# Performance work log

Measured on AMD Instinct MI355X. Metric: run time of the kernel, lower is better.

Reference implementation:

```python
import jax, jax.numpy as jnp
import numpy as np

INPUT_DIM = 1024; HID = 512; DSTATE = 64; EXPAND = 2; HDIM = 32; NHEAD = 8; DFF = 1024
DIN = EXPAND * HID          # 1024 inner dim
NH = DIN // HDIM            # 32 heads
G = 1; DCONV = 4            # ngroups, depthwise conv kernel
CONV_DIM = DIN + 2 * G * DSTATE          # 1152 (x, B, C go through conv)
DPROJ = 2 * DIN + 2 * G * DSTATE + NH    # 2208 (z, xBC, dt)
B = 2; L = 4096


def rmsnorm(x, w, eps=1e-5):
    return x * jax.lax.rsqrt(jnp.mean(x * x, axis=-1, keepdims=True) + eps) * w


def layernorm(x, w, b, eps=1e-5):
    m = jnp.mean(x, axis=-1, keepdims=True)
    v = jnp.mean((x - m) ** 2, axis=-1, keepdims=True)
    return (x - m) * jax.lax.rsqrt(v + eps) * w + b


def mamba_block(x, Wi, cw, cb, dtb, Alog, Dp, nw, Wo):
    # Mamba-2 style selective scan block (SISO, ngroups=1)
    Bb, Ln, _ = x.shape
    zxbcdt = x @ Wi                                   # [B,L,DPROJ]
    z = zxbcdt[..., :DIN]
    xBC = zxbcdt[..., DIN:DIN + CONV_DIM]
    dt = zxbcdt[..., DIN + CONV_DIM:]                 # [B,L,NH]
    # causal depthwise conv1d + silu
    xBC = jnp.transpose(xBC, (0, 2, 1))               # [B,C,L]
    xBC = jax.lax.conv_general_dilated(xBC, cw, (1,), [(DCONV - 1, 0)],
                                       feature_group_count=CONV_DIM) + cb[None, :, None]
    xBC = jax.nn.silu(jnp.transpose(xBC, (0, 2, 1)))
    xs = xBC[..., :DIN].reshape(Bb, Ln, NH, HDIM)     # [B,L,H,P]
    Bm = xBC[..., DIN:DIN + DSTATE]                   # [B,L,N]
    Cm = xBC[..., DIN + DSTATE:]                      # [B,L,N]
    dt = jax.nn.softplus(dt + dtb)                    # [B,L,H]
    decay = jnp.exp(dt * (-jnp.exp(Alog)))            # [B,L,H]
    dtx = dt[..., None] * xs                          # [B,L,H,P]

    def step(h, inp):
        dec, dx, Bt, Ct = inp                         # [B,H],[B,H,P],[B,N],[B,N]
        h = h * dec[:, :, None, None] + dx[..., None] * Bt[:, None, None, :]
        return h, jnp.einsum('bhpn,bn->bhp', h, Ct)

    h0 = jnp.zeros((Bb, NH, HDIM, DSTATE), x.dtype)
    _, ys = jax.lax.scan(step, h0, (jnp.moveaxis(decay, 1, 0), jnp.moveaxis(dtx, 1, 0),
                                    jnp.moveaxis(Bm, 1, 0), jnp.moveaxis(Cm, 1, 0)))
    y = jnp.moveaxis(ys, 0, 1) + Dp[None, None, :, None] * xs
    y = y.reshape(Bb, Ln, DIN)
    return rmsnorm(y * jax.nn.silu(z), nw) @ Wo       # gated RMSNorm + out proj


def transformer_layer(x, Wqkv, bqkv, Wo, bo, W1, b1, W2, b2, ln1w, ln1b, ln2w, ln2b):
    Bb, Ln, Dm = x.shape
    hd = Dm // NHEAD
    qkv = x @ Wqkv + bqkv
    q, k, v = jnp.split(qkv, 3, axis=-1)
    sp = lambda t: t.reshape(Bb, Ln, NHEAD, hd).transpose(0, 2, 1, 3)
    q, k, v = sp(q), sp(k), sp(v)
    att = jax.nn.softmax(jnp.einsum('bhqd,bhkd->bhqk', q, k) / np.float32(np.sqrt(hd)), axis=-1)
    o = jnp.einsum('bhqk,bhkd->bhqd', att, v).transpose(0, 2, 1, 3).reshape(Bb, Ln, Dm)
    x = layernorm(x + o @ Wo + bo, ln1w, ln1b)
    ff = jax.nn.gelu(x @ W1 + b1, approximate=False) @ W2 + b2
    return layernorm(x + ff, ln2w, ln2b)


def setup_inputs() -> dict:
    key = jax.random.key(0)
    ks = iter(jax.random.split(key, 64))
    w = lambda shape, s=0.02: jax.random.normal(next(ks), shape, jnp.float32) * s
    d = {}
    d['x'] = jax.random.normal(next(ks), (B, L, INPUT_DIM), jnp.float32)
    d['Wp'] = w((INPUT_DIM, HID)); d['bp'] = jnp.zeros((HID,), jnp.float32)
    for p in ('m1', 'm2'):
        d[p + '_Wi'] = w((HID, DPROJ))
        d[p + '_cw'] = w((CONV_DIM, 1, DCONV), 0.2)
        d[p + '_cb'] = jnp.zeros((CONV_DIM,), jnp.float32)
        d[p + '_dtb'] = jnp.log(jnp.expm1(jax.random.uniform(next(ks), (NH,), jnp.float32, 0.001, 0.1)))
        d[p + '_Alog'] = jnp.log(jax.random.uniform(next(ks), (NH,), jnp.float32, 1.0, 16.0))
        d[p + '_D'] = jnp.ones((NH,), jnp.float32)
        d[p + '_nw'] = jnp.ones((DIN,), jnp.float32)
        d[p + '_Wo'] = w((DIN, HID))
    d['n1_w'] = jnp.ones((HID,), jnp.float32); d['n2_w'] = jnp.ones((HID,), jnp.float32)
    d['ds_w'] = w((HID, HID, 3)); d['ds_b'] = jnp.zeros((HID,), jnp.float32)
    d['t_Wqkv'] = w((HID, 3 * HID)); d['t_bqkv'] = jnp.zeros((3 * HID,), jnp.float32)
    d['t_Wo'] = w((HID, HID)); d['t_bo'] = jnp.zeros((HID,), jnp.float32)
    d['t_W1'] = w((HID, DFF)); d['t_b1'] = jnp.zeros((DFF,), jnp.float32)
    d['t_W2'] = w((DFF, HID)); d['t_b2'] = jnp.zeros((HID,), jnp.float32)
    d['t_ln1w'] = jnp.ones((HID,), jnp.float32); d['t_ln1b'] = jnp.zeros((HID,), jnp.float32)
    d['t_ln2w'] = jnp.ones((HID,), jnp.float32); d['t_ln2b'] = jnp.zeros((HID,), jnp.float32)
    d['on_w'] = jnp.ones((HID,), jnp.float32); d['on_b'] = jnp.zeros((HID,), jnp.float32)
    return d


def reference(x, Wp, bp,
              m1_Wi, m1_cw, m1_cb, m1_dtb, m1_Alog, m1_D, m1_nw, m1_Wo,
              m2_Wi, m2_cw, m2_cb, m2_dtb, m2_Alog, m2_D, m2_nw, m2_Wo,
              n1_w, n2_w, ds_w, ds_b,
              t_Wqkv, t_bqkv, t_Wo, t_bo, t_W1, t_b1, t_W2, t_b2,
              t_ln1w, t_ln1b, t_ln2w, t_ln2b, on_w, on_b):
    x = x @ Wp + bp
    x = rmsnorm(mamba_block(x, m1_Wi, m1_cw, m1_cb, m1_dtb, m1_Alog, m1_D, m1_nw, m1_Wo) + x, n1_w)
    x = rmsnorm(mamba_block(x, m2_Wi, m2_cw, m2_cb, m2_dtb, m2_Alog, m2_D, m2_nw, m2_Wo) + x, n2_w)
    xt = jnp.transpose(x, (0, 2, 1))                  # [B,HID,L]
    xt = jax.lax.conv_general_dilated(xt, ds_w, (2,), [(1, 1)]) + ds_b[None, :, None]
    x = jnp.transpose(xt, (0, 2, 1))                  # [B,L/2,HID]
    x = transformer_layer(x, t_Wqkv, t_bqkv, t_Wo, t_bo, t_W1, t_b1, t_W2, t_b2,
                          t_ln1w, t_ln1b, t_ln2w, t_ln2b)
    return layernorm(x, on_w, on_b)
```

## Files before the change

### kernel.cpp

```cpp
#include <hip/hip_runtime.h>
#include <math.h>

#define DIN_   1024
#define DSTATE_ 64
#define NH_    32
#define HDIM_  32
#define CONVD_ 1152
#define DPROJ_ 2208
#define HID_   512
#define LSEQ_  4096
#define BB_    2
#define LT_    2048
#define NHEAD_ 8
#define HD_    64
#define DFF_   1024
#define LC_    256
#define NC_    16
#define NS_    4
#define KTS_   (LT_ / 64 / NS_)

typedef __attribute__((ext_vector_type(8))) short bf16x8;
typedef __attribute__((ext_vector_type(4))) short s16x4;
typedef __attribute__((ext_vector_type(4))) float f32x4;

__device__ __forceinline__ float siluf(float x) { return x / (1.f + __expf(-x)); }

__device__ __forceinline__ short f2b(float f) {
  union { float f; unsigned u; } v; v.f = f;
  unsigned r = (v.u + 0x7fffu + ((v.u >> 16) & 1u)) >> 16;
  return (short)r;
}

__device__ __forceinline__ short f2bt(float f) {
  union { float f; unsigned u; } v; v.f = f;
  return (short)(v.u >> 16);
}

__device__ __forceinline__ float b2f(short s) {
  union { unsigned u; float f; } v; v.u = ((unsigned)(unsigned short)s) << 16;
  return v.f;
}

__device__ __forceinline__ void gload16(const short* g, short* lds_base) {
#if __has_builtin(__builtin_amdgcn_global_load_lds)
  __builtin_amdgcn_global_load_lds((const __attribute__((address_space(1))) void*)g,
                                   (__attribute__((address_space(3))) void*)lds_base, 16, 0, 0);
#else
  int l = threadIdx.x & 63;
  ((bf16x8*)lds_base)[l] = *(const bf16x8*)g;
#endif
}

__device__ __forceinline__ void xcd_swz(int& bx, int& by, int& bz) {
  int nbx = gridDim.x, nby = gridDim.y;
  int nwg = nbx * nby * gridDim.z;
  int orig = (blockIdx.z * nby + blockIdx.y) * nbx + blockIdx.x;
  int q = nwg >> 3, r = nwg & 7;
  int xcd = orig & 7, lin = orig >> 3;
  int wg = (xcd < r ? xcd * (q + 1) : r * (q + 1) + (xcd - r) * q) + lin;
  bx = wg % nbx; wg /= nbx;
  by = wg % nby;
  bz = wg / nby;
}

__global__ void ec_f2b(const float* __restrict__ in, short* __restrict__ out, int n8)
{
  int i = blockIdx.x * 256 + threadIdx.x;
  if (i >= n8) return;
  const float4* p = (const float4*)(in + (size_t)i * 8);
  float4 a = p[0], b = p[1];
  bf16x8 o;
  o[0] = f2b(a.x); o[1] = f2b(a.y); o[2] = f2b(a.z); o[3] = f2b(a.w);
  o[4] = f2b(b.x); o[5] = f2b(b.y); o[6] = f2b(b.z); o[7] = f2b(b.w);
  *(bf16x8*)(out + (size_t)i * 8) = o;
}

__global__ __launch_bounds__(256) void ec_w2bt(const float* __restrict__ W,
                                               short* __restrict__ Wt, int K, int N)
{
  __shared__ float t[32][33];
  int k0 = blockIdx.x * 32, n0 = blockIdx.y * 32;
  int tx = threadIdx.x & 31, ty = threadIdx.x >> 5;
#pragma unroll
  for (int i = 0; i < 32; i += 8) t[ty + i][tx] = W[(size_t)(k0 + ty + i) * N + n0 + tx];
  __syncthreads();
#pragma unroll
  for (int i = 0; i < 32; i += 8) Wt[(size_t)(n0 + ty + i) * K + k0 + tx] = f2b(t[tx][ty + i]);
}

__global__ void ec_dswt(const float* __restrict__ w, short* __restrict__ wt)
{
  int idx = blockIdx.x * 256 + threadIdx.x;
  if (idx >= HID_ * 1536) return;
  int o = idx / 1536, r = idx % 1536;
  int k = r >> 9, i = r & 511;
  wt[idx] = f2b(w[((size_t)o * HID_ + i) * 3 + k]);
}

__global__ void ec_cwt(const float* __restrict__ cw, float* __restrict__ cwt)
{
  int idx = blockIdx.x * 256 + threadIdx.x;
  if (idx >= CONVD_ * 4) return;
  int j = idx / CONVD_, c = idx % CONVD_;
  cwt[idx] = cw[c * 4 + j];
}

__global__ __launch_bounds__(256) void ec_gemm16b(
    const short* __restrict__ A, const short* __restrict__ Wt,
    const float* __restrict__ bias, const float* __restrict__ res,
    float* __restrict__ Cf, short* __restrict__ Ch,
    int M, int N, int K, int act, int lda, long Az, int Mz)
{
  __shared__ short As_[2][4096];
  __shared__ short Bs_[2][4096];
  int bxi, byi, bzi;
  xcd_swz(bxi, byi, bzi);
  A += (size_t)bzi * Az;
  const int mz = bzi * Mz;
  const int tid = threadIdx.x;
  const int l = tid & 63, w = tid >> 6;
  const int m0 = byi * 64, n0 = bxi * 64;
  const int wm = (w >> 1) * 32, wn = (w & 1) * 32;
  const int lr = l & 15, lk = l >> 4;
  const int srow = w * 8 + (l >> 3);
  const int scol = ((l & 7) ^ (l >> 3)) * 8;
  const int rs0 = ((0 * 4 + lk) ^ (lr & 7)) * 8;
  const int rs1 = ((1 * 4 + lk) ^ (lr & 7)) * 8;

  f32x4 acc[2][2];
#pragma unroll
  for (int i = 0; i < 2; ++i)
#pragma unroll
    for (int j = 0; j < 2; ++j) acc[i][j] = f32x4{0.f, 0.f, 0.f, 0.f};

#pragma unroll
  for (int q = 0; q < 2; ++q) {
    int r = q * 32 + srow;
    const short* ga = A + (size_t)(m0 + r) * lda + scol;
    int rb = n0 + r; if (rb > N - 1) rb = N - 1;
    const short* gb = Wt + (size_t)rb * K + scol;
    gload16(ga, &As_[0][(q * 32 + w * 8) * 64]);
    gload16(gb, &Bs_[0][(q * 32 + w * 8) * 64]);
  }

  const int KT = K >> 6;
  for (int kt = 0; kt < KT; ++kt) {
    __syncthreads();
    if (kt + 1 < KT) {
      int k0 = (kt + 1) << 6;
      int nb = (kt + 1) & 1;
#pragma unroll
      for (int q = 0; q < 2; ++q) {
        int r = q * 32 + srow;
        const short* ga = A + (size_t)(m0 + r) * lda + k0 + scol;
        int rb = n0 + r; if (rb > N - 1) rb = N - 1;
        const short* gb = Wt + (size_t)rb * K + k0 + scol;
        gload16(ga, &As_[nb][(q * 32 + w * 8) * 64]);
        gload16(gb, &Bs_[nb][(q * 32 + w * 8) * 64]);
      }
    }
    int cb = kt & 1;
#pragma unroll
    for (int ksub = 0; ksub < 2; ++ksub) {
      const int rs = ksub ? rs1 : rs0;
      bf16x8 af[2], bfv[2];
#pragma unroll
      for (int mf = 0; mf < 2; ++mf)
        af[mf] = *(const bf16x8*)&As_[cb][(wm + mf * 16 + lr) * 64 + rs];
#pragma unroll
      for (int nf = 0; nf < 2; ++nf)
        bfv[nf] = *(const bf16x8*)&Bs_[cb][(wn + nf * 16 + lr) * 64 + rs];
#pragma unroll
      for (int mf = 0; mf < 2; ++mf)
#pragma unroll
        for (int nf = 0; nf < 2; ++nf)
          acc[mf][nf] = __builtin_amdgcn_mfma_f32_16x16x32_bf16(af[mf], bfv[nf], acc[mf][nf], 0, 0, 0);
    }
  }

#pragma unroll
  for (int mf = 0; mf < 2; ++mf)
#pragma unroll
    for (int nf = 0; nf < 2; ++nf)
#pragma unroll
      for (int r = 0; r < 4; ++r) {
        int m = mz + m0 + wm + mf * 16 + lk * 4 + r;
        int n = n0 + wn + nf * 16 + lr;
        if (n < N) {
          float v = acc[mf][nf][r];
          if (bias) v += bias[n];
          if (act == 1) v = 0.5f * v * (1.f + erff(v * 0.70710678118f));
          else if (act == 2 && n < HID_) v *= 0.125f;
          if (res) v += res[(size_t)m * N + n];
          if (Cf) Cf[(size_t)m * N + n] = v;
          if (Ch) Ch[(size_t)m * N + n] = f2b(v);
        }
      }
}

static inline void gemm16b(hipStream_t s, const short* A, const short* Wt, const float* bias,
                           const float* res, float* Cf, short* Ch, int M, int N, int K, int act) {
  dim3 g((N + 63) / 64, M / 64), b(256);
  ec_gemm16b<<<g, b, 0, s>>>(A, Wt, bias, res, Cf, Ch, M, N, K, act, K, 0, 0);
}

__global__ __launch_bounds__(512) void ec_dsfix(
    const short* __restrict__ x16, const short* __restrict__ wt,
    const float* __restrict__ bias, float* __restrict__ dsf, short* __restrict__ ds16)
{
  const int b = blockIdx.x, o = threadIdx.x;
  float v = bias[o];
#pragma unroll
  for (int k = 1; k < 3; ++k) {
    const short* xr = x16 + ((size_t)b * LSEQ_ + (k - 1)) * HID_;
    const short* wr = wt + (size_t)o * 1536 + k * 512;
    for (int i = 0; i < 512; i += 4) {
      s16x4 xv = *(const s16x4*)(xr + i);
      s16x4 wv = *(const s16x4*)(wr + i);
      v += b2f(xv[0]) * b2f(wv[0]) + b2f(xv[1]) * b2f(wv[1])
         + b2f(xv[2]) * b2f(wv[2]) + b2f(xv[3]) * b2f(wv[3]);
    }
  }
  dsf[(size_t)b * LT_ * HID_ + o] = v;
  ds16[(size_t)b * LT_ * HID_ + o] = f2b(v);
}

__global__ __launch_bounds__(256) void ec_conv1d_silu(
    const short* __restrict__ zx16, const float* __restrict__ cwt,
    const float* __restrict__ cb, short* __restrict__ xbc16,
    short* __restrict__ B16, short* __restrict__ C16)
{
  int idx = blockIdx.x * 256 + threadIdx.x;
  const int NG = CONVD_ / 4;
  if (idx >= BB_ * LSEQ_ * NG) return;
  int cg = idx % NG;
  int row = idx / NG;
  int l = row & (LSEQ_ - 1);
  int c0 = cg * 4;
  float4 cbv = *(const float4*)(cb + c0);
  float a0 = cbv.x, a1 = cbv.y, a2 = cbv.z, a3 = cbv.w;
#pragma unroll
  for (int j = 0; j < 4; ++j) {
    int ll = l - 3 + j;
    if (ll >= 0) {
      s16x4 xv = *(const s16x4*)(zx16 + (size_t)(row + ll - l) * DPROJ_ + DIN_ + c0);
      float4 wv = *(const float4*)(cwt + j * CONVD_ + c0);
      a0 += b2f(xv[0]) * wv.x;
      a1 += b2f(xv[1]) * wv.y;
      a2 += b2f(xv[2]) * wv.z;
      a3 += b2f(xv[3]) * wv.w;
    }
  }
  a0 = siluf(a0); a1 = siluf(a1); a2 = siluf(a2); a3 = siluf(a3);
  s16x4 pk; pk[0] = f2b(a0); pk[1] = f2b(a1); pk[2] = f2b(a2); pk[3] = f2b(a3);
  *(s16x4*)(xbc16 + (size_t)row * CONVD_ + c0) = pk;
  if (c0 >= DIN_) {
    int col = c0 - DIN_;
    if (col < 64) *(s16x4*)(B16 + (size_t)row * 64 + col) = pk;
    else          *(s16x4*)(C16 + (size_t)row * 64 + col - 64) = pk;
  }
}

__global__ __launch_bounds__(256) void ec_ssd_cumsum(
    const short* __restrict__ zx16, const float* __restrict__ dtb,
    const float* __restrict__ Alog, float* __restrict__ dts,
    float* __restrict__ lp, float* __restrict__ Pc)
{
  const int c = blockIdx.x, b = blockIdx.y, hg = blockIdx.z;
  const int t = threadIdx.x;
  const int lane = t & 63, wv = t >> 6;
  const size_t row = (size_t)b * LSEQ_ + (size_t)c * LC_ + t;
  const int h0 = hg * 8;
  __shared__ float wsum[4][8];

  bf16x8 dv = *(const bf16x8*)(zx16 + row * DPROJ_ + (DIN_ + CONVD_) + h0);
  float dt[8], cs[8];
#pragma unroll
  for (int j = 0; j < 8; ++j) {
    float x = b2f(dv[j]) + dtb[h0 + j];
    float sp = (x > 20.f) ? x : log1pf(__expf(x));
    dt[j] = sp;
    cs[j] = sp;
  }
#pragma unroll
  for (int d = 1; d < 64; d <<= 1) {
#pragma unroll
    for (int j = 0; j < 8; ++j) {
      float o = __shfl_up(cs[j], d, 64);
      if (lane >= d) cs[j] += o;
    }
  }
  if (lane == 63)
#pragma unroll
    for (int j = 0; j < 8; ++j) wsum[wv][j] = cs[j];
  __syncthreads();
#pragma unroll
  for (int j = 0; j < 8; ++j) {
    float base = 0.f;
#pragma unroll
    for (int k = 0; k < 3; ++k) if (k < wv) base += wsum[k][j];
    cs[j] += base;
  }
#pragma unroll
  for (int j = 0; j < 8; ++j) {
    int h = h0 + j;
    float lpv = -expf(Alog[h]) * cs[j];
    dts[row * NH_ + h] = dt[j];
    lp[row * NH_ + h] = lpv;
    if (t == LC_ - 1) Pc[(b * NC_ + c) * NH_ + h] = expf(lpv);
  }
}

__global__ __launch_bounds__(64) void ec_vt(
    const short* __restrict__ xbc16, const float* __restrict__ dts, short* __restrict__ VT)
{
  const int h = blockIdx.x, c = blockIdx.y, b = blockIdx.z;
  const int l = threadIdx.x;
  const size_t rowB = (size_t)b * LSEQ_ + (size_t)c * LC_;
  const size_t vtbase = (size_t)((b * NC_ + c) * NH_ + h) * 32;
  __shared__ float tile[32][33];
  for (int tt = 0; tt < 8; ++tt) {
#pragma unroll
    for (int i = 0; i < 16; ++i) {
      int r = i * 2 + (l >> 5);
      size_t row = rowB + tt * 32 + r;
      tile[r][l & 31] = b2f(xbc16[row * CONVD_ + h * 32 + (l & 31)]) * dts[row * NH_ + h];
    }
    __syncthreads();
#pragma unroll
    for (int j = 0; j < 16; ++j) {
      int p = j * 2 + (l >> 5);
      VT[(vtbase + p) * 256 + tt * 32 + (l & 31)] = f2b(tile[l & 31][p]);
    }
    __syncthreads();
  }
}

__device__ __forceinline__ float* state_ptr(float* stbuf, int b, int c, int h, int e)
{
  return stbuf + ((size_t)((b * NC_ + c) * NH_ + h)) * 2048 + e;
}

__global__ __launch_bounds__(64) void ec_ssd_p1(
    const short* __restrict__ B16, const short* __restrict__ VT,
    const float* __restrict__ lp, float* __restrict__ stbuf)
{
  const int h = blockIdx.x, c = blockIdx.y, b = blockIdx.z;
  const int l = threadIdx.x, lr = l & 15, lk = l >> 4;
  const size_t rowB = (size_t)b * LSEQ_ + (size_t)c * LC_;
  const size_t vtbase = (size_t)((b * NC_ + c) * NH_ + h) * 32;
  __shared__ short BT[64][264];
  for (int i = 0; i < 4; ++i) {
    int t = i * 64 + l;
#pragma unroll
    for (int g = 0; g < 8; ++g) {
      bf16x8 v = *(const bf16x8*)&B16[(rowB + t) * 64 + g * 8];
#pragma unroll
      for (int j = 0; j < 8; ++j) BT[g * 8 + j][t] = v[j];
    }
  }
  __syncthreads();
  const float lpE = lp[(rowB + LC_ - 1) * NH_ + h];
  f32x4 acc[2][4];
#pragma unroll
  for (int i = 0; i < 2; ++i)
#pragma unroll
    for (int j = 0; j < 4; ++j) acc[i][j] = f32x4{0.f, 0.f, 0.f, 0.f};

  for (int ks = 0; ks < 8; ++ks) {
    float wv[8];
#pragma unroll
    for (int j = 0; j < 8; ++j) {
      int t = ks * 32 + lk * 8 + j;
      wv[j] = __expf(lpE - lp[(rowB + t) * NH_ + h]);
    }
    bf16x8 af[2];
#pragma unroll
    for (int mf = 0; mf < 2; ++mf) {
      bf16x8 v = *(const bf16x8*)&VT[(vtbase + mf * 16 + lr) * 256 + ks * 32 + lk * 8];
#pragma unroll
      for (int j = 0; j < 8; ++j) af[mf][j] = f2b(b2f(v[j]) * wv[j]);
    }
#pragma unroll
    for (int nf = 0; nf < 4; ++nf) {
      bf16x8 bf = *(const bf16x8*)&BT[nf * 16 + lr][ks * 32 + lk * 8];
#pragma unroll
      for (int mf = 0; mf < 2; ++mf)
        acc[mf][nf] = __builtin_amdgcn_mfma_f32_16x16x32_bf16(af[mf], bf, acc[mf][nf], 0, 0, 0);
    }
  }
#pragma unroll
  for (int mf = 0; mf < 2; ++mf)
#pragma unroll
    for (int nf = 0; nf < 4; ++nf)
#pragma unroll
      for (int r = 0; r < 4; ++r) {
        int p = mf * 16 + lk * 4 + r, n = nf * 16 + lr;
        *state_ptr(stbuf, b, c, h, p * 64 + n) = acc[mf][nf][r];
      }
}

__global__ __launch_bounds__(512) void ec_scan_p2(
    float* __restrict__ stbuf, const float* __restrict__ Pc)
{
  const int h = blockIdx.x, b = blockIdx.y;
  const int tid = threadIdx.x;
  const int e = (tid >> 4) * 64 + (tid & 15) * 4;
  float h0 = 0.f, h1 = 0.f, h2 = 0.f, h3 = 0.f;
  for (int c = 0; c < NC_; ++c) {
    float* ptr = state_ptr(stbuf, b, c, h, e);
    float4 S = *(float4*)ptr;
    *(float4*)ptr = make_float4(h0, h1, h2, h3);
    float P = Pc[(b * NC_ + c) * NH_ + h];
    h0 = h0 * P + S.x;
    h1 = h1 * P + S.y;
    h2 = h2 * P + S.z;
    h3 = h3 * P + S.w;
  }
}

__global__ __launch_bounds__(256) void ec_ssd_p3(
    const short* __restrict__ B16, const short* __restrict__ C16,
    const short* __restrict__ VT, const float* __restrict__ lp,
    const short* __restrict__ xbc16, const float* __restrict__ Dp,
    float* __restrict__ stbuf, short* __restrict__ y16)
{
  const int h = blockIdx.x, c = blockIdx.y, b = blockIdx.z;
  const int tid = threadIdx.x;
  const int w = tid >> 6, l = tid & 63, lr = l & 15, lk = l >> 4;
  const size_t rowB = (size_t)b * LSEQ_ + (size_t)c * LC_;
  const size_t vtbase = (size_t)((b * NC_ + c) * NH_ + h) * 32;
  __shared__ short hI[32][72];
  __shared__ short Pl[4][64][72];

  for (int i = tid; i < 2048; i += 256)
    hI[i >> 6][i & 63] = f2b(*state_ptr(stbuf, b, c, h, i));
  __syncthreads();

  const int t0 = w * 64;
  bf16x8 cf[4][2];
#pragma unroll
  for (int tf = 0; tf < 4; ++tf)
#pragma unroll
    for (int ks = 0; ks < 2; ++ks)
      cf[tf][ks] = *(const bf16x8*)&C16[(rowB + t0 + tf * 16 + lr) * 64 + ks * 32 + lk * 8];

  f32x4 Y[4][2];
#pragma unroll
  for (int i = 0; i < 4; ++i)
#pragma unroll
    for (int j = 0; j < 2; ++j) Y[i][j] = f32x4{0.f, 0.f, 0.f, 0.f};
#pragma unroll
  for (int nf = 0; nf < 2; ++nf)
#pragma unroll
    for (int ks = 0; ks < 2; ++ks) {
      bf16x8 hf = *(const bf16x8*)&hI[nf * 16 + lr][ks * 32 + lk * 8];
#pragma unroll
      for (int mf = 0; mf < 4; ++mf)
        Y[mf][nf] = __builtin_amdgcn_mfma_f32_16x16x32_bf16(cf[mf][ks], hf, Y[mf][nf], 0, 0, 0);
    }
#pragma unroll
  for (int mf = 0; mf < 4; ++mf)
#pragma unroll
    for (int r = 0; r < 4; ++r) {
      float e = __expf(lp[(rowB + t0 + mf * 16 + lk * 4 + r) * NH_ + h]);
      Y[mf][0][r] *= e;
      Y[mf][1][r] *= e;
    }
  float tlp[4];
#pragma unroll
  for (int tf = 0; tf < 4; ++tf)
    tlp[tf] = lp[(rowB + t0 + tf * 16 + lr) * NH_ + h];

  for (int st = 0; st <= w; ++st) {
    const int s0 = st * 64;
#pragma unroll
    for (int half = 0; half < 2; ++half) {
      f32x4 ST[2][4];
#pragma unroll
      for (int i = 0; i < 2; ++i)
#pragma unroll
        for (int j = 0; j < 4; ++j) ST[i][j] = f32x4{0.f, 0.f, 0.f, 0.f};
#pragma unroll
      for (int sf2 = 0; sf2 < 2; ++sf2) {
        int sf = half * 2 + sf2;
#pragma unroll
        for (int ks = 0; ks < 2; ++ks) {
          bf16x8 bfr = *(const bf16x8*)&B16[(rowB + s0 + sf * 16 + lr) * 64 + ks * 32 + lk * 8];
#pragma unroll
          for (int tf = 0; tf < 4; ++tf)
            ST[sf2][tf] = __builtin_amdgcn_mfma_f32_16x16x32_bf16(bfr, cf[tf][ks], ST[sf2][tf], 0, 0, 0);
        }
      }
#pragma unroll
      for (int sf2 = 0; sf2 < 2; ++sf2) {
        int sf = half * 2 + sf2;
        float slp[4];
#pragma unroll
        for (int r = 0; r < 4; ++r)
          slp[r] = lp[(rowB + s0 + sf * 16 + lk * 4 + r) * NH_ + h];
#pragma unroll
        for (int tf = 0; tf < 4; ++tf) {
          float pv[4];
#pragma unroll
          for (int r = 0; r < 4; ++r) {
            pv[r] = ST[sf2][tf][r] * __expf(tlp[tf] - slp[r]);
            if (st == w && (sf * 16 + lk * 4 + r) > (tf * 16 + lr)) pv[r] = 0.f;
          }
          union { float f; unsigned u; } q0, q1, q2, q3;
          q0.f = pv[0]; q1.f = pv[1]; q2.f = pv[2]; q3.f = pv[3];
          uint2 pk;
          pk.x = (q0.u >> 16) | (q1.u & 0xffff0000u);
          pk.y = (q2.u >> 16) | (q3.u & 0xffff0000u);
          *(uint2*)&Pl[w][tf * 16 + lr][sf * 16 + lk * 4] = pk;
        }
      }
    }
    __builtin_amdgcn_sched_barrier(0);
    asm volatile("s_waitcnt lgkmcnt(0)" ::: "memory");
    __builtin_amdgcn_sched_barrier(0);
#pragma unroll
    for (int ks = 0; ks < 2; ++ks) {
      bf16x8 vf[2];
#pragma unroll
      for (int nf = 0; nf < 2; ++nf)
        vf[nf] = *(const bf16x8*)&VT[(vtbase + nf * 16 + lr) * 256 + s0 + ks * 32 + lk * 8];
#pragma unroll
      for (int mf = 0; mf < 4; ++mf) {
        bf16x8 pf = *(const bf16x8*)&Pl[w][mf * 16 + lr][ks * 32 + lk * 8];
#pragma unroll
        for (int nf = 0; nf < 2; ++nf)
          Y[mf][nf] = __builtin_amdgcn_mfma_f32_16x16x32_bf16(pf, vf[nf], Y[mf][nf], 0, 0, 0);
      }
    }
  }
  const float Dh = Dp[h];
#pragma unroll
  for (int mf = 0; mf < 4; ++mf)
#pragma unroll
    for (int r = 0; r < 4; ++r) {
      size_t yrow = rowB + t0 + mf * 16 + lk * 4 + r;
#pragma unroll
      for (int nf = 0; nf < 2; ++nf) {
        float xv = b2f(xbc16[yrow * CONVD_ + h * 32 + nf * 16 + lr]);
        y16[yrow * DIN_ + h * 32 + nf * 16 + lr] = f2b(Y[mf][nf][r] + Dh * xv);
      }
    }
}

__global__ __launch_bounds__(256) void ec_gate_rms16(
    const short* __restrict__ y16, const short* __restrict__ zx16,
    const float* __restrict__ nw, short* __restrict__ out)
{
  const int row = blockIdx.x;
  const int c0 = threadIdx.x * 4;
  s16x4 yv = *(const s16x4*)(y16 + (size_t)row * DIN_ + c0);
  s16x4 zv = *(const s16x4*)(zx16 + (size_t)row * DPROJ_ + c0);
  float v[4]; float ss = 0.f;
#pragma unroll
  for (int j = 0; j < 4; ++j) {
    float t = b2f(yv[j]) * siluf(b2f(zv[j]));
    v[j] = t; ss += t * t;
  }
#pragma unroll
  for (int m = 32; m >= 1; m >>= 1) ss += __shfl_xor(ss, m, 64);
  __shared__ float buf[4];
  if ((threadIdx.x & 63) == 0) buf[threadIdx.x >> 6] = ss;
  __syncthreads();
  ss = buf[0] + buf[1] + buf[2] + buf[3];
  float scale = rsqrtf(ss / (float)DIN_ + 1e-5f);
  float4 wv = *(const float4*)(nw + c0);
  s16x4 ov;
  ov[0] = f2b(v[0] * scale * wv.x);
  ov[1] = f2b(v[1] * scale * wv.y);
  ov[2] = f2b(v[2] * scale * wv.z);
  ov[3] = f2b(v[3] * scale * wv.w);
  *(s16x4*)(out + (size_t)row * DIN_ + c0) = ov;
}

__global__ __launch_bounds__(128) void ec_rmsadd16(
    const short* __restrict__ a16, const float* __restrict__ bres,
    const float* __restrict__ w, float* __restrict__ out, short* __restrict__ out16)
{
  const int row = blockIdx.x;
  const int c0 = threadIdx.x * 4;
  s16x4 av = *(const s16x4*)(a16 + (size_t)row * HID_ + c0);
  float4 brv = *(const float4*)(bres + (size_t)row * HID_ + c0);
  float v[4]; float ss = 0.f;
  v[0] = b2f(av[0]) + brv.x; v[1] = b2f(av[1]) + brv.y;
  v[2] = b2f(av[2]) + brv.z; v[3] = b2f(av[3]) + brv.w;
#pragma unroll
  for (int j = 0; j < 4; ++j) ss += v[j] * v[j];
#pragma unroll
  for (int m = 32; m >= 1; m >>= 1) ss += __shfl_xor(ss, m, 64);
  __shared__ float buf[2];
  if ((threadIdx.x & 63) == 0) buf[threadIdx.x >> 6] = ss;
  __syncthreads();
  ss = buf[0] + buf[1];
  float scale = rsqrtf(ss / (float)HID_ + 1e-5f);
  float4 wv = *(const float4*)(w + c0);
  float o0 = v[0] * scale * wv.x, o1 = v[1] * scale * wv.y;
  float o2 = v[2] * scale * wv.z, o3 = v[3] * scale * wv.w;
  *(float4*)(out + (size_t)row * HID_ + c0) = make_float4(o0, o1, o2, o3);
  s16x4 ov; ov[0] = f2b(o0); ov[1] = f2b(o1); ov[2] = f2b(o2); ov[3] = f2b(o3);
  *(s16x4*)(out16 + (size_t)row * HID_ + c0) = ov;
}

__global__ __launch_bounds__(128) void ec_ln16(
    const float* __restrict__ in, const float* __restrict__ w,
    const float* __restrict__ bb, float* __restrict__ out, short* __restrict__ out16)
{
  const int row = blockIdx.x;
  const float* ir = in + (size_t)row * HID_;
  float v[4]; float s = 0.f, s2 = 0.f;
#pragma unroll
  for (int j = 0; j < 4; ++j) {
    int c = j * 128 + threadIdx.x;
    float t = ir[c];
    v[j] = t; s += t; s2 += t * t;
  }
#pragma unroll
  for (int m = 32; m >= 1; m >>= 1) { s += __shfl_xor(s, m, 64); s2 += __shfl_xor(s2, m, 64); }
  __shared__ float buf[4];
  if ((threadIdx.x & 63) == 0) { int wi = threadIdx.x >> 6; buf[wi * 2] = s; buf[wi * 2 + 1] = s2; }
  __syncthreads();
  s = buf[0] + buf[2]; s2 = buf[1] + buf[3];
  float mean = s / (float)HID_;
  float var = s2 / (float)HID_ - mean * mean;
  float inv = rsqrtf(var + 1e-5f);
#pragma unroll
  for (int j = 0; j < 4; ++j) {
    int c = j * 128 + threadIdx.x;
    float o = (v[j] - mean) * inv * w[c] + bb[c];
    out[(size_t)row * HID_ + c] = o;
    if (out16) out16[(size_t)row * HID_ + c] = f2b(o);
  }
}

__global__ __launch_bounds__(512) void ec_attn16(
    const short* __restrict__ qkv, short* __restrict__ Op, float2* __restrict__ ml)
{
  const int b = blockIdx.z & 1, split = blockIdx.z >> 1;
  const int h = blockIdx.y, qt = blockIdx.x;
  __shared__ short Kl[64 * 68];
  __shared__ short Vl[64 * 68];
  __shared__ short Pl[128 * 68];
  const int tid = threadIdx.x;
  const int l = tid & 63, w = tid >> 6;
  const int lr = l & 15, lk = l >> 4;

  const size_t qrow = (size_t)b * LT_ + qt * 128 + w * 16 + lr;
  bf16x8 qf[2];
  qf[0] = *(const bf16x8*)&qkv[qrow * 1536 + h * HD_ + lk * 8];
  qf[1] = *(const bf16x8*)&qkv[qrow * 1536 + h * HD_ + lk * 8 + 32];

  float mrun[4] = {-1e30f, -1e30f, -1e30f, -1e30f};
  float lsum[4] = {0.f, 0.f, 0.f, 0.f};
  f32x4 O[4];
#pragma unroll
  for (int df = 0; df < 4; ++df) O[df] = f32x4{0.f, 0.f, 0.f, 0.f};

  const int krow = tid >> 3, kcg = (tid & 7) * 8;
  const int vd = tid & 63, vw = tid >> 6;

  for (int kt = split * KTS_; kt < (split + 1) * KTS_; ++kt) {
    const size_t krbase = (size_t)b * LT_ + kt * 64;
    {
      const short* kp = &qkv[(krbase + krow) * 1536 + HID_ + h * HD_ + kcg];
      *(bf16x8*)&Kl[krow * 68 + kcg] = *(const bf16x8*)kp;
    }
#pragma unroll
    for (int kk = 0; kk < 2; ++kk) {
      int key0 = vw * 8 + kk * 4;
      s16x4 pk;
#pragma unroll
      for (int j = 0; j < 4; ++j)
        pk[j] = qkv[(krbase + key0 + j) * 1536 + 2 * HID_ + h * HD_ + vd];
      *(s16x4*)&Vl[vd * 68 + key0] = pk;
    }
    __syncthreads();

    f32x4 S[4];
#pragma unroll
    for (int nf = 0; nf < 4; ++nf) S[nf] = f32x4{0.f, 0.f, 0.f, 0.f};
#pragma unroll
    for (int ks = 0; ks < 2; ++ks)
#pragma unroll
      for (int nf = 0; nf < 4; ++nf) {
        bf16x8 kb = *(const bf16x8*)&Kl[(nf * 16 + lr) * 68 + ks * 32 + lk * 8];
        S[nf] = __builtin_amdgcn_mfma_f32_16x16x32_bf16(qf[ks], kb, S[nf], 0, 0, 0);
      }

    int ok = 1;
#pragma unroll
    for (int nf = 0; nf < 4; ++nf)
#pragma unroll
      for (int r = 0; r < 4; ++r)
        ok &= (S[nf][r] <= mrun[r] + 8.f);
    if (!__all(ok)) {
      float fr[4];
#pragma unroll
      for (int r = 0; r < 4; ++r) {
        float mt = fmaxf(fmaxf(S[0][r], S[1][r]), fmaxf(S[2][r], S[3][r]));
        mt = fmaxf(mt, __shfl_xor(mt, 1));
        mt = fmaxf(mt, __shfl_xor(mt, 2));
        mt = fmaxf(mt, __shfl_xor(mt, 4));
        mt = fmaxf(mt, __shfl_xor(mt, 8));
        float mn = fmaxf(mrun[r], mt);
        fr[r] = __expf(mrun[r] - mn);
        mrun[r] = mn;
        lsum[r] *= fr[r];
      }
#pragma unroll
      for (int df = 0; df < 4; ++df) {
        O[df][0] *= fr[0]; O[df][1] *= fr[1]; O[df][2] *= fr[2]; O[df][3] *= fr[3];
      }
    }
#pragma unroll
    for (int nf = 0; nf < 4; ++nf)
#pragma unroll
      for (int r = 0; r < 4; ++r) {
        float p = __expf(S[nf][r] - mrun[r]);
        lsum[r] += p;
        Pl[(w * 16 + lk * 4 + r) * 68 + nf * 16 + lr] = f2bt(p);
      }

#pragma unroll
    for (int ks = 0; ks < 2; ++ks) {
      bf16x8 pa = *(const bf16x8*)&Pl[(w * 16 + lr) * 68 + ks * 32 + lk * 8];
#pragma unroll
      for (int df = 0; df < 4; ++df) {
        bf16x8 vb = *(const bf16x8*)&Vl[(df * 16 + lr) * 68 + ks * 32 + lk * 8];
        O[df] = __builtin_amdgcn_mfma_f32_16x16x32_bf16(pa, vb, O[df], 0, 0, 0);
      }
    }
    __syncthreads();
  }

#pragma unroll
  for (int r = 0; r < 4; ++r) {
    lsum[r] += __shfl_xor(lsum[r], 1);
    lsum[r] += __shfl_xor(lsum[r], 2);
    lsum[r] += __shfl_xor(lsum[r], 4);
    lsum[r] += __shfl_xor(lsum[r], 8);
  }
  const size_t sstride = (size_t)BB_ * NHEAD_ * LT_;
  const size_t obase = (size_t)split * sstride + ((size_t)b * NHEAD_ + h) * LT_ + qt * 128 + w * 16;
#pragma unroll
  for (int df = 0; df < 4; ++df)
#pragma unroll
    for (int r = 0; r < 4; ++r)
      Op[(obase + lk * 4 + r) * 64 + df * 16 + lr] = f2b(O[df][r]);
  if (lr == 0)
#pragma unroll
    for (int r = 0; r < 4; ++r)
      ml[obase + lk * 4 + r] = make_float2(mrun[r], lsum[r]);
}

__global__ __launch_bounds__(256) void ec_attn_comb(
    const short* __restrict__ Op, const float2* __restrict__ ml, short* __restrict__ out)
{
  const int qt = blockIdx.x, h = blockIdx.y, b = blockIdx.z;
  const int r = threadIdx.x >> 2, c0 = (threadIdx.x & 3) * 16;
  const int qrow = qt * 64 + r;
  const size_t sstride = (size_t)BB_ * NHEAD_ * LT_;
  const size_t rb = ((size_t)b * NHEAD_ + h) * LT_ + qrow;
  float m[NS_], lv[NS_];
  float mmax = -1e30f;
#pragma unroll
  for (int s = 0; s < NS_; ++s) {
    float2 v = ml[rb + s * sstride];
    m[s] = v.x; lv[s] = v.y;
    mmax = fmaxf(mmax, m[s]);
  }
  float den = 0.f, wsc[NS_];
#pragma unroll
  for (int s = 0; s < NS_; ++s) { wsc[s] = __expf(m[s] - mmax); den += lv[s] * wsc[s]; }
  float inv = 1.f / den;
  float o[16];
#pragma unroll
  for (int i = 0; i < 16; ++i) o[i] = 0.f;
#pragma unroll
  for (int s = 0; s < NS_; ++s) {
    const short* p = Op + (rb + s * sstride) * 64 + c0;
    float wq = wsc[s];
#pragma unroll
    for (int i = 0; i < 4; ++i) {
      s16x4 v = *(const s16x4*)(p + i * 4);
      o[i * 4 + 0] += b2f(v[0]) * wq; o[i * 4 + 1] += b2f(v[1]) * wq;
      o[i * 4 + 2] += b2f(v[2]) * wq; o[i * 4 + 3] += b2f(v[3]) * wq;
    }
  }
  short* op = out + ((size_t)b * LT_ + qrow) * HID_ + h * HD_ + c0;
#pragma unroll
  for (int i = 0; i < 16; ++i) op[i] = f2b(o[i] * inv);
}

extern "C" void kernel_launch(void* const* d_in, const int* in_sizes, int n_in,
                              void* d_out, int out_size, void* d_ws, size_t ws_size,
                              hipStream_t stream)
{
  const float* x_in   = (const float*)d_in[0];
  const float* Wp     = (const float*)d_in[1];
  const float* bp     = (const float*)d_in[2];
  const float* m_Wi[2]   = {(const float*)d_in[3],  (const float*)d_in[11]};
  const float* m_cw[2]   = {(const float*)d_in[4],  (const float*)d_in[12]};
  const float* m_cb[2]   = {(const float*)d_in[5],  (const float*)d_in[13]};
  const float* m_dtb[2]  = {(const float*)d_in[6],  (const float*)d_in[14]};
  const float* m_Alog[2] = {(const float*)d_in[7],  (const float*)d_in[15]};
  const float* m_D[2]    = {(const float*)d_in[8],  (const float*)d_in[16]};
  const float* m_nw[2]   = {(const float*)d_in[9],  (const float*)d_in[17]};
  const float* m_Wo[2]   = {(const float*)d_in[10], (const float*)d_in[18]};
  const float* n_w[2]    = {(const float*)d_in[19], (const float*)d_in[20]};
  const float* ds_w   = (const float*)d_in[21];
  const float* ds_b   = (const float*)d_in[22];
  const float* t_Wqkv = (const float*)d_in[23];
  const float* t_bqkv = (const float*)d_in[24];
  const float* t_Wo   = (const float*)d_in[25];
  const float* t_bo   = (const float*)d_in[26];
  const float* t_W1   = (const float*)d_in[27];
  const float* t_b1   = (const float*)d_in[28];
  const float* t_W2   = (const float*)d_in[29];
  const float* t_b2   = (const float*)d_in[30];
  const float* t_ln1w = (const float*)d_in[31];
  const float* t_ln1b = (const float*)d_in[32];
  const float* t_ln2w = (const float*)d_in[33];
  const float* t_ln2b = (const float*)d_in[34];
  const float* on_w   = (const float*)d_in[35];
  const float* on_b   = (const float*)d_in[36];

  char* ws = (char*)d_ws;
  float* bx    = (float*)(ws + 0);
  short* zx16  = (short*)(ws + 16777216);
  float* stbuf = (float*)(ws + 16777216 + 36175872);
  short* xbc16 = (short*)(ws + 89128960);
  short* y16   = (short*)(ws + 126877696);
  short* VT    = (short*)(ws + 143654912);
  float* lp    = (float*)(ws + 160432128);
  float* dts   = (float*)(ws + 161480704);
  short* wslot = (short*)(ws + 162529280);
  float* Pc    = (float*)(ws + 165150720);
  float* cwt   = (float*)(ws + 165154816);

  short* B16 = wslot;
  short* C16 = wslot + 524288;
  short* a16buf = (short*)(ws + 126877696);

  short* x16     = (short*)(ws + 126877696);
  short* bx16    = (short*)(ws + 89128960);
  short* gated16 = (short*)(ws + 89128960 + 18874368);

  short*  Opart = (short*)(ws + 89128960);
  float2* mlbuf = (float2*)(ws + 89128960 + 33554432);

  char* tzone = ws + 16777216;
  short* ds16  = (short*)tzone;
  float* dsf   = (float*)(tzone + 4194304);
  short* qkv16 = (short*)(tzone + 12582912);
  short* att16 = (short*)(tzone + 25165824);
  float* bt1   = (float*)(tzone + 29360128);
  short* ln116 = (short*)(tzone + 37748736);
  float* bxt2  = (float*)(tzone + 41943040);
  short* ff16  = (short*)(tzone + 50331648);
  float* bt2   = (float*)(tzone + 58720256);
  float* bxt3  = (float*)(ws + 89128960);

  const int MR = BB_ * LSEQ_;
  const int MT = BB_ * LT_;

  ec_f2b<<<(MR * 1024 / 8 + 255) / 256, 256, 0, stream>>>(x_in, x16, MR * 1024 / 8);
  ec_w2bt<<<dim3(1024 / 32, 512 / 32), 256, 0, stream>>>(Wp, wslot, 1024, 512);
  gemm16b(stream, x16, wslot, bp, nullptr, bx, bx16, MR, HID_, 1024, 0);

  for (int blk = 0; blk < 2; ++blk) {
    ec_w2bt<<<dim3(512 / 32, 2208 / 32), 256, 0, stream>>>(m_Wi[blk], wslot, 512, 2208);
    gemm16b(stream, bx16, wslot, nullptr, nullptr, nullptr, zx16, MR, DPROJ_, HID_, 0);
    ec_cwt<<<(CONVD_ * 4 + 255) / 256, 256, 0, stream>>>(m_cw[blk], cwt);
    ec_conv1d_silu<<<(MR * (CONVD_ / 4) + 255) / 256, 256, 0, stream>>>(
        zx16, cwt, m_cb[blk], xbc16, B16, C16);
    ec_ssd_cumsum<<<dim3(NC_, BB_, NH_ / 8), 256, 0, stream>>>(zx16, m_dtb[blk], m_Alog[blk], dts, lp, Pc);
    ec_vt<<<dim3(NH_, NC_, BB_), 64, 0, stream>>>(xbc16, dts, VT);
    ec_ssd_p1<<<dim3(NH_, NC_, BB_), 64, 0, stream>>>(B16, VT, lp, stbuf);
    ec_scan_p2<<<dim3(NH_, BB_), 512, 0, stream>>>(stbuf, Pc);
    ec_ssd_p3<<<dim3(NH_, NC_, BB_), 256, 0, stream>>>(B16, C16, VT, lp, xbc16, m_D[blk], stbuf, y16);
    ec_gate_rms16<<<MR, 256, 0, stream>>>(y16, zx16, m_nw[blk], gated16);
    ec_w2bt<<<dim3(1024 / 32, 512 / 32), 256, 0, stream>>>(m_Wo[blk], wslot, 1024, 512);
    gemm16b(stream, gated16, wslot, nullptr, nullptr, nullptr, a16buf, MR, HID_, DIN_, 0);
    ec_rmsadd16<<<MR, 128, 0, stream>>>(a16buf, bx, n_w[blk], bx, bx16);
  }

  ec_dswt<<<(HID_ * 1536 + 255) / 256, 256, 0, stream>>>(ds_w, wslot);
  {
    dim3 g(512 / 64, LT_ / 64, BB_), b(256);
    ec_gemm16b<<<g, b, 0, stream>>>(bx16 - 512, wslot, ds_b, nullptr, dsf, ds16,
                                    LT_, HID_, 1536, 0, 1024, (long)LSEQ_ * HID_, LT_);
  }
  ec_dsfix<<<BB_, 512, 0, stream>>>(bx16, wslot, ds_b, dsf, ds16);

  ec_w2bt<<<dim3(512 / 32, 1536 / 32), 256, 0, stream>>>(t_Wqkv, wslot, 512, 1536);
  gemm16b(stream, ds16, wslot, t_bqkv, nullptr, nullptr, qkv16, MT, 3 * HID_, HID_, 2);
  ec_attn16<<<dim3(LT_ / 128, NHEAD_, BB_ * NS_), 512, 0, stream>>>(qkv16, Opart, mlbuf);
  ec_attn_comb<<<dim3(LT_ / 64, NHEAD_, BB_), 256, 0, stream>>>(Opart, mlbuf, att16);
  ec_w2bt<<<dim3(512 / 32, 512 / 32), 256, 0, stream>>>(t_Wo, wslot, 512, 512);
  gemm16b(stream, att16, wslot, t_bo, dsf, bt1, nullptr, MT, HID_, HID_, 0);
  ec_ln16<<<MT, 128, 0, stream>>>(bt1, t_ln1w, t_ln1b, bxt2, ln116);
  ec_w2bt<<<dim3(512 / 32, 1024 / 32), 256, 0, stream>>>(t_W1, wslot, 512, 1024);
  gemm16b(stream, ln116, wslot, t_b1, nullptr, nullptr, ff16, MT, DFF_, HID_, 1);
  ec_w2bt<<<dim3(1024 / 32, 512 / 32), 256, 0, stream>>>(t_W2, wslot, 1024, 512);
  gemm16b(stream, ff16, wslot, t_b2, bxt2, bt2, nullptr, MT, HID_, DFF_, 0);
  ec_ln16<<<MT, 128, 0, stream>>>(bt2, t_ln2w, t_ln2b, bxt3, nullptr);
  ec_ln16<<<MT, 128, 0, stream>>>(bxt3, on_w, on_b, (float*)d_out, nullptr);
}
```

Measured before the change: 576.0 us.

## Write V pre-transposed from QKV GEMM and double-buffer K/V tiles in attention

The QKV GEMM epilogue now writes the V columns to a separate pre-transposed, tiled buffer (64x64 tiles per batch/head). This lets attention load V with a single vector load per thread instead of strided scalar gathers. Attention also double-buffers the K and V shared-memory tiles, staging the next tile while the current one is computed. The cost is an extra workspace buffer and more shared memory per block, which may lower occupancy. It also relies on loop-end synchronisation to make the double buffering safe.

New measurement: 573.6 us. No clear change (-0.4%).

```diff
diff --git a/kernel.cpp b/kernel.cpp
--- a/kernel.cpp
+++ b/kernel.cpp
@@ -108,7 +108,7 @@
 __global__ __launch_bounds__(256) void ec_gemm16b(
     const short* __restrict__ A, const short* __restrict__ Wt,
     const float* __restrict__ bias, const float* __restrict__ res,
-    float* __restrict__ Cf, short* __restrict__ Ch,
+    float* __restrict__ Cf, short* __restrict__ Ch, short* __restrict__ Cv,
     int M, int N, int K, int act, int lda, long Az, int Mz)
 {
   __shared__ short As_[2][4096];
@@ -178,6 +178,26 @@
     }
   }
 
+  if (Cv && act == 2 && n0 >= 2 * HID_) {
+    const int hh = (n0 - 2 * HID_) >> 6;
+#pragma unroll
+    for (int mf = 0; mf < 2; ++mf) {
+      int mrow = m0 + wm + mf * 16 + lk * 4;
+      int bb = mrow >> 11, tt = mrow & (LT_ - 1);
+      size_t tb = (((size_t)(bb * NHEAD_ + hh) * (LT_ / 64) + (tt >> 6)) << 12) + (tt & 63);
+#pragma unroll
+      for (int nf = 0; nf < 2; ++nf) {
+        int d = wn + nf * 16 + lr;
+        float bv = bias ? bias[n0 + d] : 0.f;
+        s16x4 ov;
+#pragma unroll
+        for (int r = 0; r < 4; ++r) ov[r] = f2b(acc[mf][nf][r] + bv);
+        *(s16x4*)&Cv[tb + (size_t)d * 64] = ov;
+      }
+    }
+    return;
+  }
+
 #pragma unroll
   for (int mf = 0; mf < 2; ++mf)
 #pragma unroll
@@ -201,7 +221,7 @@
 static inline void gemm16b(hipStream_t s, const short* A, const short* Wt, const float* bias,
                            const float* res, float* Cf, short* Ch, int M, int N, int K, int act) {
   dim3 g((N + 63) / 64, M / 64), b(256);
-  ec_gemm16b<<<g, b, 0, s>>>(A, Wt, bias, res, Cf, Ch, M, N, K, act, K, 0, 0);
+  ec_gemm16b<<<g, b, 0, s>>>(A, Wt, bias, res, Cf, Ch, nullptr, M, N, K, act, K, 0, 0);
 }
 
 __global__ __launch_bounds__(512) void ec_dsfix(
@@ -638,12 +658,13 @@
 }
 
 __global__ __launch_bounds__(512) void ec_attn16(
-    const short* __restrict__ qkv, short* __restrict__ Op, float2* __restrict__ ml)
+    const short* __restrict__ qkv, const short* __restrict__ vt16,
+    short* __restrict__ Op, float2* __restrict__ ml)
 {
   const int b = blockIdx.z & 1, split = blockIdx.z >> 1;
   const int h = blockIdx.y, qt = blockIdx.x;
-  __shared__ short Kl[64 * 68];
-  __shared__ short Vl[64 * 68];
+  __shared__ short Kl[2][64 * 68];
+  __shared__ short Vl[2][64 * 68];
   __shared__ short Pl[128 * 68];
   const int tid = threadIdx.x;
   const int l = tid & 63, w = tid >> 6;
@@ -661,24 +682,24 @@
   for (int df = 0; df < 4; ++df) O[df] = f32x4{0.f, 0.f, 0.f, 0.f};
 
   const int krow = tid >> 3, kcg = (tid & 7) * 8;
-  const int vd = tid & 63, vw = tid >> 6;
-
-  for (int kt = split * KTS_; kt < (split + 1) * KTS_; ++kt) {
+  const short* vtile = vt16 + (size_t)(b * NHEAD_ + h) * (LT_ / 64) * 4096;
+  const int vofs = tid * 8;
+  const int vlds = (tid >> 3) * 68 + (tid & 7) * 8;
+
+  auto stageKV = [&](int kt, int bufi) {
     const size_t krbase = (size_t)b * LT_ + kt * 64;
-    {
-      const short* kp = &qkv[(krbase + krow) * 1536 + HID_ + h * HD_ + kcg];
-      *(bf16x8*)&Kl[krow * 68 + kcg] = *(const bf16x8*)kp;
-    }
-#pragma unroll
-    for (int kk = 0; kk < 2; ++kk) {
-      int key0 = vw * 8 + kk * 4;
-      s16x4 pk;
-#pragma unroll
-      for (int j = 0; j < 4; ++j)
-        pk[j] = qkv[(krbase + key0 + j) * 1536 + 2 * HID_ + h * HD_ + vd];
-      *(s16x4*)&Vl[vd * 68 + key0] = pk;
-    }
-    __syncthreads();
+    const short* kp = &qkv[(krbase + krow) * 1536 + HID_ + h * HD_ + kcg];
+    *(bf16x8*)&Kl[bufi][krow * 68 + kcg] = *(const bf16x8*)kp;
+    bf16x8 vv = *(const bf16x8*)&vtile[(size_t)kt * 4096 + vofs];
+    *(bf16x8*)&Vl[bufi][vlds] = vv;
+  };
+
+  stageKV(split * KTS_, 0);
+  __syncthreads();
+
+  for (int i = 0; i < KTS_; ++i) {
+    const int cur = i & 1;
+    if (i + 1 < KTS_) stageKV(split * KTS_ + i + 1, cur ^ 1);
 
     f32x4 S[4];
 #pragma unroll
@@ -687,7 +708,7 @@
     for (int ks = 0; ks < 2; ++ks)
 #pragma unroll
       for (int nf = 0; nf < 4; ++nf) {
-        bf16x8 kb = *(const bf16x8*)&Kl[(nf * 16 + lr) * 68 + ks * 32 + lk * 8];
+        bf16x8 kb = *(const bf16x8*)&Kl[cur][(nf * 16 + lr) * 68 + ks * 32 + lk * 8];
         S[nf] = __builtin_amdgcn_mfma_f32_16x16x32_bf16(qf[ks], kb, S[nf], 0, 0, 0);
       }
 
@@ -730,7 +751,7 @@
       bf16x8 pa = *(const bf16x8*)&Pl[(w * 16 + lr) * 68 + ks * 32 + lk * 8];
 #pragma unroll
       for (int df = 0; df < 4; ++df) {
-        bf16x8 vb = *(const bf16x8*)&Vl[(df * 16 + lr) * 68 + ks * 32 + lk * 8];
+        bf16x8 vb = *(const bf16x8*)&Vl[cur][(df * 16 + lr) * 68 + ks * 32 + lk * 8];
         O[df] = __builtin_amdgcn_mfma_f32_16x16x32_bf16(pa, vb, O[df], 0, 0, 0);
       }
     }
@@ -863,6 +884,7 @@
   float* bxt2  = (float*)(tzone + 41943040);
   short* ff16  = (short*)(tzone + 50331648);
   float* bt2   = (float*)(tzone + 58720256);
+  short* vt16  = (short*)(tzone + 67108864);
   float* bxt3  = (float*)(ws + 89128960);
 
   const int MR = BB_ * LSEQ_;
@@ -892,14 +914,18 @@
   ec_dswt<<<(HID_ * 1536 + 255) / 256, 256, 0, stream>>>(ds_w, wslot);
   {
     dim3 g(512 / 64, LT_ / 64, BB_), b(256);
-    ec_gemm16b<<<g, b, 0, stream>>>(bx16 - 512, wslot, ds_b, nullptr, dsf, ds16,
+    ec_gemm16b<<<g, b, 0, stream>>>(bx16 - 512, wslot, ds_b, nullptr, dsf, ds16, nullptr,
                                     LT_, HID_, 1536, 0, 1024, (long)LSEQ_ * HID_, LT_);
   }
   ec_dsfix<<<BB_, 512, 0, stream>>>(bx16, wslot, ds_b, dsf, ds16);
 
   ec_w2bt<<<dim3(512 / 32, 1536 / 32), 256, 0, stream>>>(t_Wqkv, wslot, 512, 1536);
-  gemm16b(stream, ds16, wslot, t_bqkv, nullptr, nullptr, qkv16, MT, 3 * HID_, HID_, 2);
-  ec_attn16<<<dim3(LT_ / 128, NHEAD_, BB_ * NS_), 512, 0, stream>>>(qkv16, Opart, mlbuf);
+  {
+    dim3 g(1536 / 64, MT / 64), b(256);
+    ec_gemm16b<<<g, b, 0, stream>>>(ds16, wslot, t_bqkv, nullptr, nullptr, qkv16, vt16,
+                                    MT, 3 * HID_, HID_, 2, HID_, 0, 0);
+  }
+  ec_attn16<<<dim3(LT_ / 128, NHEAD_, BB_ * NS_), 512, 0, stream>>>(qkv16, vt16, Opart, mlbuf);
   ec_attn_comb<<<dim3(LT_ / 64, NHEAD_, BB_), 256, 0, stream>>>(Opart, mlbuf, att16);
   ec_w2bt<<<dim3(512 / 32, 512 / 32), 256, 0, stream>>>(t_Wo, wslot, 512, 512);
   gemm16b(stream, att16, wslot, t_bo, dsf, bt1, nullptr, MT, HID_, HID_, 0);
```
